# Kernel tuning notes

Measured on AMD Instinct MI355X. Metric: run time of the kernel, lower is better.

Reference implementation:

```python
import jax, jax.numpy as jnp
import numpy as np

B, T, D, H = 8, 1024, 512, 8
CH = D // H          # chunk_size = d_model // num_heads
PAD = 0              # pad_token_id
MAX_TRANS = 1024     # translen cap from source
NINF = float('-inf')


def setup_inputs() -> dict:
    key = jax.random.key(0)
    ks = jax.random.split(key, 8)
    features = jax.random.normal(ks[0], (B, T, D), jnp.float32)
    pos_embed = jax.random.normal(ks[1], (B, T, D), jnp.float32)
    tokens = jax.random.randint(ks[2], (B, T), 0, 32000, dtype=jnp.int32)
    Wq = jax.random.normal(ks[3], (D, 2 * D), jnp.float32) * 0.02
    bq = jnp.zeros((D,), jnp.float32)
    Wk = jax.random.normal(ks[4], (D, 2 * D), jnp.float32) * 0.02
    bk = jnp.zeros((D,), jnp.float32)
    Wg = jax.random.normal(ks[5], (H, 2 * D), jnp.float32) * 0.02
    bg = jnp.zeros((H,), jnp.float32)
    return dict(features=features, pos_embed=pos_embed, tokens=tokens,
                Wq=Wq, bq=bq, Wk=Wk, bk=bk, Wg=Wg, bg=bg)


def _safe_log_softmax(x, axis):
    # matches torch F.log_softmax followed by re-masking: rows that are all -inf stay -inf
    m = jnp.max(x, axis=axis, keepdims=True)
    allinf = jnp.isneginf(m)
    m_safe = jnp.where(allinf, 0.0, m)
    lse = m_safe + jnp.log(jnp.sum(jnp.exp(x - m_safe), axis=axis, keepdims=True))
    lse = jnp.where(allinf, 0.0, lse)
    return x - lse


def _safe_logsumexp(x, axis):
    # matches the custom logsumexp helper in the source (all -inf -> -inf, no nan)
    m = jnp.max(x, axis=axis)
    mask = jnp.isneginf(m)
    m_safe = jnp.where(mask, 0.0, m)
    s = jnp.sum(jnp.exp(x - jnp.expand_dims(m_safe, axis)), axis=axis)
    return jnp.log(jnp.where(mask, 1.0, s)) + jnp.where(mask, NINF, m_safe)


def reference(features, pos_embed, tokens, Wq, bq, Wk, bk, Wg, bg):
    # features_withpos = cat(decoder_out, link positional embedding)  -> [B, T, 2D]
    f = jnp.concatenate([features, pos_embed], axis=-1)
    q = (f @ Wq.T + bq).reshape(B, T, H, CH)
    k = (f @ Wk.T + bk).reshape(B, T, H, CH)
    log_gates = jax.nn.log_softmax(f @ Wg.T + bg, axis=-1)  # [B, T, H]
    # einsum 'bicf,bjcf->bijc' with c = head chunk
    scores = jnp.einsum('bihc,bjhc->bijh', q, k) / np.float32(np.sqrt(CH))  # [B,T,T,H]

    translen = min(MAX_TRANS, T - 1)
    n_valid = jnp.sum(tokens != PAD, axis=-1)  # [B]
    # banded indices: position i links to positions i+1 .. i+translen
    band_idx = jnp.arange(T)[:, None] + jnp.arange(translen)[None, :] + 1  # [T, translen]
    invalid = band_idx[None, :, :] >= n_valid[:, None, None]               # [B, T, translen]
    idx_c = jnp.where(invalid, 0, band_idx[None, :, :])
    idx_full = jnp.broadcast_to(idx_c[..., None], (B, T, translen, H))
    extract = jnp.take_along_axis(scores, idx_full, axis=2)                # [B,T,translen,H]
    extract = jnp.where(invalid[..., None], NINF, extract)
    # normalize over transition axis, then mask fully-invalid rows back to -inf
    extract = _safe_log_softmax(extract, axis=2)
    nouse = jnp.all(invalid, axis=-1)                                      # [B, T]
    extract = jnp.where(nouse[:, :, None, None], NINF, extract)
    # head-gated logsumexp over heads -> banded links [B, T, translen]
    links_band = _safe_logsumexp(extract + log_gates[:, :, None, :], axis=-1)
    # restore_valid_links: scatter band back to full [B, T, T] (-inf elsewhere)
    rel = jnp.arange(T)[None, :] - jnp.arange(T)[:, None] - 1              # [T, T]
    valid = (rel >= 0) & (rel < translen)
    rel_c = jnp.clip(rel, 0, translen - 1)
    rel_full = jnp.broadcast_to(rel_c[None, :, :], (B, T, T))
    out = jnp.take_along_axis(links_band, rel_full, axis=2)
    return jnp.where(valid[None, :, :], out, NINF)
```

## Files before the change

### kernel.cpp

```cpp
#include <hip/hip_runtime.h>
#include <math.h>

#define BATCH 8
#define T 1024
#define NH 8
#define NROW 8192
#define NEG_INF (-INFINITY)
#define SENT (-1.0e30f)
#define SC 0.180336880f
#define LOG2E 1.442695041f

typedef __attribute__((ext_vector_type(8))) short short8;
typedef __attribute__((ext_vector_type(4))) float f32x4;

__device__ __forceinline__ ushort f2bf(float x) {
  uint u = __float_as_uint(x);
  return (ushort)((u + 0x7FFFu + ((u >> 16) & 1u)) >> 16);
}
__device__ __forceinline__ uint pack2(float a, float b) {
  return (uint)f2bf(a) | ((uint)f2bf(b) << 16);
}
__device__ __forceinline__ void gl_lds16(const ushort* g, ushort* l) {
  __builtin_amdgcn_global_load_lds(
      (const __attribute__((address_space(1))) unsigned int*)g,
      (__attribute__((address_space(3))) unsigned int*)l, 16, 0, 0);
}

__global__ __launch_bounds__(256) void k_prep(
    const float* __restrict__ feat, const float* __restrict__ pos,
    const int* __restrict__ tokens,
    const float* __restrict__ Wq, const float* __restrict__ Wk,
    const float* __restrict__ Wg, const float* __restrict__ bg,
    ushort* __restrict__ fbf, ushort* __restrict__ Wbf,
    float* __restrict__ gout, int* __restrict__ nvout) {
  const int bid = blockIdx.x;
  const int tid = threadIdx.x;

  if (bid < 1024) {
    __shared__ __align__(16) float Ws[8192];
#pragma unroll
    for (int u = 0; u < 8; ++u)
      ((float4*)Ws)[u * 256 + tid] = ((const float4*)Wg)[u * 256 + tid];
    __syncthreads();

    const int w = tid >> 6, l = tid & 63;
    const int c0 = l * 16;
    const int row0 = bid * 8 + w * 2;

    float4 f[2][4];
#pragma unroll
    for (int r = 0; r < 2; ++r) {
      const int row = row0 + r;
      const float* src = (c0 < 512) ? (feat + (size_t)row * 512 + c0)
                                    : (pos + (size_t)row * 512 + (c0 - 512));
#pragma unroll
      for (int q4 = 0; q4 < 4; ++q4) f[r][q4] = *(const float4*)(src + q4 * 4);
      uint4 o0, o1;
      o0.x = pack2(f[r][0].x, f[r][0].y); o0.y = pack2(f[r][0].z, f[r][0].w);
      o0.z = pack2(f[r][1].x, f[r][1].y); o0.w = pack2(f[r][1].z, f[r][1].w);
      o1.x = pack2(f[r][2].x, f[r][2].y); o1.y = pack2(f[r][2].z, f[r][2].w);
      o1.z = pack2(f[r][3].x, f[r][3].y); o1.w = pack2(f[r][3].z, f[r][3].w);
      *(uint4*)(fbf + (size_t)row * 1024 + c0) = o0;
      *(uint4*)(fbf + (size_t)row * 1024 + c0 + 8) = o1;
    }

    float s[2][8];
#pragma unroll
    for (int h = 0; h < 8; ++h) {
      const float* wg = Ws + h * 1024 + c0;
      float4 w0 = *(const float4*)(wg + 0);
      float4 w1 = *(const float4*)(wg + 4);
      float4 w2 = *(const float4*)(wg + 8);
      float4 w3 = *(const float4*)(wg + 12);
#pragma unroll
      for (int r = 0; r < 2; ++r)
        s[r][h] = f[r][0].x * w0.x + f[r][0].y * w0.y + f[r][0].z * w0.z + f[r][0].w * w0.w
                + f[r][1].x * w1.x + f[r][1].y * w1.y + f[r][1].z * w1.z + f[r][1].w * w1.w
                + f[r][2].x * w2.x + f[r][2].y * w2.y + f[r][2].z * w2.z + f[r][2].w * w2.w
                + f[r][3].x * w3.x + f[r][3].y * w3.y + f[r][3].z * w3.z + f[r][3].w * w3.w;
    }
#pragma unroll
    for (int m = 1; m < 64; m <<= 1)
#pragma unroll
      for (int r = 0; r < 2; ++r)
#pragma unroll
        for (int h = 0; h < 8; ++h) s[r][h] += __shfl_xor(s[r][h], m, 64);
    if (l == 0) {
#pragma unroll
      for (int r = 0; r < 2; ++r) {
        float lg[8], mx = -1e30f;
#pragma unroll
        for (int h = 0; h < 8; ++h) { lg[h] = s[r][h] + bg[h]; mx = fmaxf(mx, lg[h]); }
        float sum = 0.f;
#pragma unroll
        for (int h = 0; h < 8; ++h) sum += __expf(lg[h] - mx);
        const float lse = mx + __logf(sum);
#pragma unroll
        for (int h = 0; h < 8; ++h) gout[(size_t)(row0 + r) * 8 + h] = lg[h] - lse;
      }
    }
  } else if (bid < 1536) {
    const int gid = (bid - 1024) * 256 + tid;
    const int e0 = gid * 8;
    const int n = e0 >> 10, k = e0 & 1023;
    const float* src = (n < 512) ? (Wq + (size_t)n * 1024 + k)
                                 : (Wk + (size_t)(n - 512) * 1024 + k);
    float4 a = *(const float4*)src;
    float4 b = *(const float4*)(src + 4);
    uint4 o;
    o.x = pack2(a.x, a.y); o.y = pack2(a.z, a.w);
    o.z = pack2(b.x, b.y); o.w = pack2(b.z, b.w);
    *(uint4*)(Wbf + (size_t)n * 1024 + k) = o;
  } else {
    const int b = bid - 1536;
    int cnt = 0;
    for (int i = tid; i < T; i += 256) cnt += (tokens[b * T + i] != 0) ? 1 : 0;
    __shared__ int s[256];
    s[tid] = cnt;
    __syncthreads();
    for (int st = 128; st > 0; st >>= 1) {
      if (tid < st) s[tid] += s[tid + st];
      __syncthreads();
    }
    if (tid == 0) nvout[b] = s[0];
  }
}

__global__ __launch_bounds__(256) void k_gemm(
    const ushort* __restrict__ fbf, const ushort* __restrict__ Wbf,
    const float* __restrict__ bq, const float* __restrict__ bk,
    ushort* __restrict__ qbuf, ushort* __restrict__ kbuf) {
  const int g = blockIdx.x + 8 * blockIdx.y;
  const int wid = (g & 7) * 64 + (g >> 3);
  const int n0 = (wid & 7) * 128;
  const int m0 = (wid >> 3) * 128;
  const int tid = threadIdx.x;
  const int w = tid >> 6, l = tid & 63;
  const int lo = l & 15, quad = l >> 4;
  const int wm0 = (w >> 1) * 64, wn0 = (w & 1) * 64;

  __shared__ ushort As[2][128 * 64];
  __shared__ ushort Bs[2][128 * 64];

  f32x4 acc[4][4];
#pragma unroll
  for (int i = 0; i < 4; ++i)
#pragma unroll
    for (int j = 0; j < 4; ++j) acc[i][j] = (f32x4){0.f, 0.f, 0.f, 0.f};

  const int c8 = (tid & 7) * 8;
  const int r0 = tid >> 3;

  auto stage = [&](int buf, int k0) {
#pragma unroll
    for (int u = 0; u < 4; ++u) {
      gl_lds16(fbf + (size_t)(m0 + u * 32 + r0) * 1024 + k0 + c8,
               As[buf] + (size_t)w * 512 + u * 2048);
      gl_lds16(Wbf + (size_t)(n0 + u * 32 + r0) * 1024 + k0 + c8,
               Bs[buf] + (size_t)w * 512 + u * 2048);
    }
  };

  stage(0, 0);
  int cur = 0;
  for (int k0 = 0; k0 < 1024; k0 += 64) {
    __syncthreads();
    if (k0 + 64 < 1024) stage(cur ^ 1, k0 + 64);
    const ushort* pA = As[cur];
    const ushort* pB = Bs[cur];
#pragma unroll
    for (int kk = 0; kk < 2; ++kk) {
      short8 af[4], bfr[4];
#pragma unroll
      for (int mi = 0; mi < 4; ++mi)
        af[mi] = *(const short8*)(pA + (size_t)(wm0 + mi * 16 + lo) * 64 + kk * 32 + quad * 8);
#pragma unroll
      for (int ni = 0; ni < 4; ++ni)
        bfr[ni] = *(const short8*)(pB + (size_t)(wn0 + ni * 16 + lo) * 64 + kk * 32 + quad * 8);
#pragma unroll
      for (int mi = 0; mi < 4; ++mi)
#pragma unroll
        for (int ni = 0; ni < 4; ++ni)
          acc[mi][ni] = __builtin_amdgcn_mfma_f32_16x16x32_bf16(bfr[ni], af[mi], acc[mi][ni], 0, 0, 0);
    }
    cur ^= 1;
  }

  float4 bias4[4];
#pragma unroll
  for (int ni = 0; ni < 4; ++ni) {
    const int gn = n0 + wn0 + ni * 16 + quad * 4;
    bias4[ni] = *(const float4*)((gn < 512) ? (bq + gn) : (bk + gn - 512));
  }
#pragma unroll
  for (int mi = 0; mi < 4; ++mi) {
    const int m = m0 + wm0 + mi * 16 + lo;
#pragma unroll
    for (int ni = 0; ni < 4; ++ni) {
      const int gn = n0 + wn0 + ni * 16 + quad * 4;
      ushort* dst = (gn < 512) ? (qbuf + (size_t)m * 512 + gn)
                               : (kbuf + (size_t)m * 512 + gn - 512);
      ushort4 o;
      o.x = f2bf(acc[mi][ni][0] + bias4[ni].x);
      o.y = f2bf(acc[mi][ni][1] + bias4[ni].y);
      o.z = f2bf(acc[mi][ni][2] + bias4[ni].z);
      o.w = f2bf(acc[mi][ni][3] + bias4[ni].w);
      *(ushort4*)dst = o;
    }
  }
}

__global__ __launch_bounds__(256) void k_pass1(
    const ushort* __restrict__ q, const ushort* __restrict__ kv,
    const float* __restrict__ g, const int* __restrict__ nvp,
    float* __restrict__ Wt) {
  const int it = blockIdx.x, h = blockIdx.y, b = blockIdx.z;
  const int nv = nvp[b];
  const int i0 = it * 64;
  const int tid = threadIdx.x;
  const int w = tid >> 6, l = tid & 63;
  const int lo = l & 15, quad = l >> 4;

  __shared__ ushort Ks[2][64 * 64];

  const int i = i0 + w * 16 + lo;
  const ushort* qp = q + (size_t)(b * T + i) * 512 + h * 64 + quad * 8;
  const short8 a0 = *(const short8*)qp;
  const short8 a1 = *(const short8*)(qp + 32);

  float lsum = 0.f;
  const int ntile = ((nv + 63) >> 6) - it;

  if (ntile > 0) {
    auto stage = [&](int buf, int jt) {
#pragma unroll
      for (int u = 0; u < 2; ++u) {
        const int s = u * 256 + tid;
        const int row = s >> 3, c = s & 7;
        gl_lds16(kv + (size_t)(b * T + jt * 64 + row) * 512 + h * 64 + ((c ^ (row & 7)) * 8),
                 Ks[buf] + (size_t)(u * 256 + w * 64) * 8);
      }
    };
    stage(0, it);
    __syncthreads();
    for (int s = 0; s < ntile; ++s) {
      if (s + 1 < ntile) stage((s + 1) & 1, it + s + 1);
      const ushort* kbase = Ks[s & 1];
      const int j0 = (it + s) * 64;
      const bool diag = (s == 0);
      const bool masked = diag | (j0 + 64 > nv);
#pragma unroll
      for (int ni = 0; ni < 4; ++ni) {
        if (diag && ni < w) continue;
        const int rw = ni * 16 + lo;
        const short8 b0 = *(const short8*)(kbase + (size_t)rw * 64 + ((quad ^ (rw & 7)) * 8));
        const short8 b1 = *(const short8*)(kbase + (size_t)rw * 64 + (((4 + quad) ^ (rw & 7)) * 8));
        f32x4 acc = (f32x4){0.f, 0.f, 0.f, 0.f};
        acc = __builtin_amdgcn_mfma_f32_16x16x32_bf16(b0, a0, acc, 0, 0, 0);
        acc = __builtin_amdgcn_mfma_f32_16x16x32_bf16(b1, a1, acc, 0, 0, 0);
        if (!masked) {
#pragma unroll
          for (int r = 0; r < 4; ++r) lsum += __builtin_amdgcn_exp2f(acc[r] * SC);
        } else {
          const int jb = j0 + ni * 16 + quad * 4;
#pragma unroll
          for (int r = 0; r < 4; ++r) {
            const int j = jb + r;
            if (j > i && j < nv) lsum += __builtin_amdgcn_exp2f(acc[r] * SC);
          }
        }
      }
      __syncthreads();
    }
  }

  lsum += __shfl_xor(lsum, 16, 64);
  lsum += __shfl_xor(lsum, 32, 64);
  if (quad == 0) {
    const size_t row = (size_t)(b * T) + i;
    Wt[(size_t)h * NROW + row] =
        (lsum > 0.f) ? (g[row * 8 + h] - __logf(lsum)) : NEG_INF;
  }
}

__global__ __launch_bounds__(256) void k_pass2(
    const ushort* __restrict__ q, const ushort* __restrict__ kv,
    const float* __restrict__ Wt, const int* __restrict__ nvp,
    float* __restrict__ out) {
  const int jt = blockIdx.x, it = blockIdx.y, b = blockIdx.z;
  const int nv = nvp[b];
  const int i0 = it * 64, j0 = jt * 64;
  const int tid = threadIdx.x;

  if (jt < it || j0 >= nv) {
    const int r0 = tid >> 4, c0 = (tid & 15) * 4;
    float4 v; v.x = v.y = v.z = v.w = SENT;
#pragma unroll
    for (int u = 0; u < 4; ++u)
      *(float4*)(out + ((size_t)(b * T + i0 + r0 + u * 16)) * T + j0 + c0) = v;
    return;
  }

  const int w = tid >> 6, l = tid & 63;
  const int lo = l & 15, quad = l >> 4;
  const int i = i0 + w * 16 + lo;

  __shared__ ushort Ks[2][64 * 64];

  auto stage = [&](int buf, int h) {
#pragma unroll
    for (int u = 0; u < 2; ++u) {
      const int s = u * 256 + tid;
      const int row = s >> 3, c = s & 7;
      gl_lds16(kv + (size_t)(b * T + j0 + row) * 512 + h * 64 + ((c ^ (row & 7)) * 8),
               Ks[buf] + (size_t)(u * 256 + w * 64) * 8);
    }
  };

  stage(0, 0);

  const ushort* qb = q + (size_t)(b * T + i) * 512 + quad * 8;
  short8 qa0[8], qa1[8];
  float wl[8];
#pragma unroll
  for (int h = 0; h < 8; ++h) {
    qa0[h] = *(const short8*)(qb + h * 64);
    qa1[h] = *(const short8*)(qb + h * 64 + 32);
    wl[h] = Wt[(size_t)h * NROW + b * T + i] * LOG2E;
  }

  float se[4][4];
#pragma unroll
  for (int a = 0; a < 4; ++a)
#pragma unroll
    for (int c = 0; c < 4; ++c) se[a][c] = 0.f;

  __syncthreads();

#pragma unroll
  for (int h = 0; h < 8; ++h) {
    if (h < 7) stage((h + 1) & 1, h + 1);
    const ushort* kbase = Ks[h & 1];
#pragma unroll
    for (int ni = 0; ni < 4; ++ni) {
      const int rw = ni * 16 + lo;
      const short8 b0 = *(const short8*)(kbase + (size_t)rw * 64 + ((quad ^ (rw & 7)) * 8));
      const short8 b1 = *(const short8*)(kbase + (size_t)rw * 64 + (((4 + quad) ^ (rw & 7)) * 8));
      f32x4 acc = (f32x4){0.f, 0.f, 0.f, 0.f};
      acc = __builtin_amdgcn_mfma_f32_16x16x32_bf16(b0, qa0[h], acc, 0, 0, 0);
      acc = __builtin_amdgcn_mfma_f32_16x16x32_bf16(b1, qa1[h], acc, 0, 0, 0);
#pragma unroll
      for (int r = 0; r < 4; ++r)
        se[ni][r] += __builtin_amdgcn_exp2f(acc[r] * SC + wl[h]);
    }
    if (h < 7) __syncthreads();
  }

  const size_t orow = ((size_t)(b * T + i)) * T;
#pragma unroll
  for (int ni = 0; ni < 4; ++ni) {
    const int jb = j0 + ni * 16 + quad * 4;
    float4 v;
    v.x = (jb + 0 > i && jb + 0 < nv) ? fmaxf(__logf(se[ni][0]), SENT) : SENT;
    v.y = (jb + 1 > i && jb + 1 < nv) ? fmaxf(__logf(se[ni][1]), SENT) : SENT;
    v.z = (jb + 2 > i && jb + 2 < nv) ? fmaxf(__logf(se[ni][2]), SENT) : SENT;
    v.w = (jb + 3 > i && jb + 3 < nv) ? fmaxf(__logf(se[ni][3]), SENT) : SENT;
    *(float4*)(out + orow + jb) = v;
  }
}

extern "C" void kernel_launch(void* const* d_in, const int* in_sizes, int n_in,
                              void* d_out, int out_size, void* d_ws, size_t ws_size,
                              hipStream_t stream) {
  (void)in_sizes; (void)n_in; (void)out_size; (void)ws_size;
  const float* feat = (const float*)d_in[0];
  const float* pos  = (const float*)d_in[1];
  const int* tokens = (const int*)d_in[2];
  const float* Wq = (const float*)d_in[3];
  const float* bq = (const float*)d_in[4];
  const float* Wk = (const float*)d_in[5];
  const float* bk = (const float*)d_in[6];
  const float* Wg = (const float*)d_in[7];
  const float* bg = (const float*)d_in[8];
  float* out = (float*)d_out;

  ushort* qbuf = (ushort*)d_ws;
  ushort* kbuf = qbuf + (size_t)NROW * 512;
  ushort* Wbf  = kbuf + (size_t)NROW * 512;
  float*  gbuf = (float*)(Wbf + (size_t)1024 * 1024);
  float*  Wt   = gbuf + (size_t)NROW * NH;
  int*    nv   = (int*)(Wt + (size_t)NH * NROW);

  ushort* fbf = (ushort*)d_out;

  k_prep<<<dim3(1544), dim3(256), 0, stream>>>(feat, pos, tokens, Wq, Wk, Wg, bg,
                                               fbf, Wbf, gbuf, nv);
  k_gemm<<<dim3(8, 64), dim3(256), 0, stream>>>(fbf, Wbf, bq, bk, qbuf, kbuf);
  k_pass1<<<dim3(16, NH, BATCH), dim3(256), 0, stream>>>(qbuf, kbuf, gbuf, nv, Wt);
  k_pass2<<<dim3(16, 16, BATCH), dim3(256), 0, stream>>>(qbuf, kbuf, Wt, nv, out);
}
```

Baseline: 182.5 us.

## Retile GEMM to 512 threads with swizzled LDS, widen pass2 tiles, reorder grids

The GEMM moves to 512 threads with 8 waves, each computing a 64x32 sub-tile, and adds an XOR swizzle on the LDS layout to avoid bank conflicts on fragment reads. Pass2 doubles the j-tile to 128 columns so each staged K tile and Q load serve more MFMAs. Q fragments are now loaded per head instead of being held for all eight heads, and an unmasked fast path handles the epilogue. Both attention grids put batch on the fastest-varying block index, which changes scheduling and load balance across the causal/valid region. The risks are more register pressure from se[8][4], coarser skipping of masked tiles, and more redundant work on diagonal tiles.

```diff
diff --git a/kernel.cpp b/kernel.cpp
--- a/kernel.cpp
+++ b/kernel.cpp
@@ -126,7 +126,7 @@
   }
 }
 
-__global__ __launch_bounds__(256) void k_gemm(
+__global__ __launch_bounds__(512, 4) void k_gemm(
     const ushort* __restrict__ fbf, const ushort* __restrict__ Wbf,
     const float* __restrict__ bq, const float* __restrict__ bk,
     ushort* __restrict__ qbuf, ushort* __restrict__ kbuf) {
@@ -137,27 +137,28 @@
   const int tid = threadIdx.x;
   const int w = tid >> 6, l = tid & 63;
   const int lo = l & 15, quad = l >> 4;
-  const int wm0 = (w >> 1) * 64, wn0 = (w & 1) * 64;
+  const int wm0 = (w >> 2) * 64;
+  const int wn0 = (w & 3) * 32;
 
   __shared__ ushort As[2][128 * 64];
   __shared__ ushort Bs[2][128 * 64];
 
-  f32x4 acc[4][4];
+  f32x4 acc[4][2];
 #pragma unroll
   for (int i = 0; i < 4; ++i)
 #pragma unroll
-    for (int j = 0; j < 4; ++j) acc[i][j] = (f32x4){0.f, 0.f, 0.f, 0.f};
-
-  const int c8 = (tid & 7) * 8;
+    for (int j = 0; j < 2; ++j) acc[i][j] = (f32x4){0.f, 0.f, 0.f, 0.f};
+
+  const int csw = ((tid & 7) ^ ((tid >> 3) & 7)) * 8;
   const int r0 = tid >> 3;
 
   auto stage = [&](int buf, int k0) {
 #pragma unroll
-    for (int u = 0; u < 4; ++u) {
-      gl_lds16(fbf + (size_t)(m0 + u * 32 + r0) * 1024 + k0 + c8,
-               As[buf] + (size_t)w * 512 + u * 2048);
-      gl_lds16(Wbf + (size_t)(n0 + u * 32 + r0) * 1024 + k0 + c8,
-               Bs[buf] + (size_t)w * 512 + u * 2048);
+    for (int u = 0; u < 2; ++u) {
+      gl_lds16(fbf + (size_t)(m0 + u * 64 + r0) * 1024 + k0 + csw,
+               As[buf] + (size_t)(u * 512 + w * 64) * 8);
+      gl_lds16(Wbf + (size_t)(n0 + u * 64 + r0) * 1024 + k0 + csw,
+               Bs[buf] + (size_t)(u * 512 + w * 64) * 8);
     }
   };
 
@@ -170,25 +171,26 @@
     const ushort* pB = Bs[cur];
 #pragma unroll
     for (int kk = 0; kk < 2; ++kk) {
-      short8 af[4], bfr[4];
+      const int swz = ((kk * 4 + quad) ^ (lo & 7)) * 8;
+      short8 af[4], bfr[2];
 #pragma unroll
       for (int mi = 0; mi < 4; ++mi)
-        af[mi] = *(const short8*)(pA + (size_t)(wm0 + mi * 16 + lo) * 64 + kk * 32 + quad * 8);
-#pragma unroll
-      for (int ni = 0; ni < 4; ++ni)
-        bfr[ni] = *(const short8*)(pB + (size_t)(wn0 + ni * 16 + lo) * 64 + kk * 32 + quad * 8);
+        af[mi] = *(const short8*)(pA + (size_t)(wm0 + mi * 16 + lo) * 64 + swz);
+#pragma unroll
+      for (int ni = 0; ni < 2; ++ni)
+        bfr[ni] = *(const short8*)(pB + (size_t)(wn0 + ni * 16 + lo) * 64 + swz);
 #pragma unroll
       for (int mi = 0; mi < 4; ++mi)
 #pragma unroll
-        for (int ni = 0; ni < 4; ++ni)
+        for (int ni = 0; ni < 2; ++ni)
           acc[mi][ni] = __builtin_amdgcn_mfma_f32_16x16x32_bf16(bfr[ni], af[mi], acc[mi][ni], 0, 0, 0);
     }
     cur ^= 1;
   }
 
-  float4 bias4[4];
-#pragma unroll
-  for (int ni = 0; ni < 4; ++ni) {
+  float4 bias4[2];
+#pragma unroll
+  for (int ni = 0; ni < 2; ++ni) {
     const int gn = n0 + wn0 + ni * 16 + quad * 4;
     bias4[ni] = *(const float4*)((gn < 512) ? (bq + gn) : (bk + gn - 512));
   }
@@ -196,7 +198,7 @@
   for (int mi = 0; mi < 4; ++mi) {
     const int m = m0 + wm0 + mi * 16 + lo;
 #pragma unroll
-    for (int ni = 0; ni < 4; ++ni) {
+    for (int ni = 0; ni < 2; ++ni) {
       const int gn = n0 + wn0 + ni * 16 + quad * 4;
       ushort* dst = (gn < 512) ? (qbuf + (size_t)m * 512 + gn)
                                : (kbuf + (size_t)m * 512 + gn - 512);
@@ -214,7 +216,7 @@
     const ushort* __restrict__ q, const ushort* __restrict__ kv,
     const float* __restrict__ g, const int* __restrict__ nvp,
     float* __restrict__ Wt) {
-  const int it = blockIdx.x, h = blockIdx.y, b = blockIdx.z;
+  const int b = blockIdx.x, h = blockIdx.y, it = blockIdx.z;
   const int nv = nvp[b];
   const int i0 = it * 64;
   const int tid = threadIdx.x;
@@ -287,53 +289,49 @@
     const ushort* __restrict__ q, const ushort* __restrict__ kv,
     const float* __restrict__ Wt, const int* __restrict__ nvp,
     float* __restrict__ out) {
-  const int jt = blockIdx.x, it = blockIdx.y, b = blockIdx.z;
+  const int b = blockIdx.x, jt = blockIdx.y, it = blockIdx.z;
   const int nv = nvp[b];
-  const int i0 = it * 64, j0 = jt * 64;
+  const int i0 = it * 64, j0 = jt * 128;
   const int tid = threadIdx.x;
 
-  if (jt < it || j0 >= nv) {
-    const int r0 = tid >> 4, c0 = (tid & 15) * 4;
+  if (j0 + 127 <= i0 || j0 >= nv) {
+    const int r0 = tid >> 5, c0 = (tid & 31) * 4;
     float4 v; v.x = v.y = v.z = v.w = SENT;
 #pragma unroll
-    for (int u = 0; u < 4; ++u)
-      *(float4*)(out + ((size_t)(b * T + i0 + r0 + u * 16)) * T + j0 + c0) = v;
+    for (int u = 0; u < 8; ++u)
+      *(float4*)(out + ((size_t)(b * T + i0 + r0 + u * 8)) * T + j0 + c0) = v;
     return;
   }
 
-  const int w = tid >> 6, l = tid & 63;
+  const int wv = tid >> 6, l = tid & 63;
   const int lo = l & 15, quad = l >> 4;
-  const int i = i0 + w * 16 + lo;
-
-  __shared__ ushort Ks[2][64 * 64];
+  const int i = i0 + wv * 16 + lo;
+
+  __shared__ ushort Ks[2][128 * 64];
 
   auto stage = [&](int buf, int h) {
 #pragma unroll
-    for (int u = 0; u < 2; ++u) {
+    for (int u = 0; u < 4; ++u) {
       const int s = u * 256 + tid;
       const int row = s >> 3, c = s & 7;
       gl_lds16(kv + (size_t)(b * T + j0 + row) * 512 + h * 64 + ((c ^ (row & 7)) * 8),
-               Ks[buf] + (size_t)(u * 256 + w * 64) * 8);
+               Ks[buf] + (size_t)(u * 256 + wv * 64) * 8);
     }
   };
 
   stage(0, 0);
 
   const ushort* qb = q + (size_t)(b * T + i) * 512 + quad * 8;
-  short8 qa0[8], qa1[8];
   float wl[8];
 #pragma unroll
-  for (int h = 0; h < 8; ++h) {
-    qa0[h] = *(const short8*)(qb + h * 64);
-    qa1[h] = *(const short8*)(qb + h * 64 + 32);
+  for (int h = 0; h < 8; ++h)
     wl[h] = Wt[(size_t)h * NROW + b * T + i] * LOG2E;
-  }
-
-  float se[4][4];
-#pragma unroll
-  for (int a = 0; a < 4; ++a)
-#pragma unroll
-    for (int c = 0; c < 4; ++c) se[a][c] = 0.f;
+
+  float se[8][4];
+#pragma unroll
+  for (int a = 0; a < 8; ++a)
+#pragma unroll
+    for (int r = 0; r < 4; ++r) se[a][r] = 0.f;
 
   __syncthreads();
 
@@ -341,14 +339,16 @@
   for (int h = 0; h < 8; ++h) {
     if (h < 7) stage((h + 1) & 1, h + 1);
     const ushort* kbase = Ks[h & 1];
-#pragma unroll
-    for (int ni = 0; ni < 4; ++ni) {
+    const short8 a0 = *(const short8*)(qb + h * 64);
+    const short8 a1 = *(const short8*)(qb + h * 64 + 32);
+#pragma unroll
+    for (int ni = 0; ni < 8; ++ni) {
       const int rw = ni * 16 + lo;
       const short8 b0 = *(const short8*)(kbase + (size_t)rw * 64 + ((quad ^ (rw & 7)) * 8));
       const short8 b1 = *(const short8*)(kbase + (size_t)rw * 64 + (((4 + quad) ^ (rw & 7)) * 8));
       f32x4 acc = (f32x4){0.f, 0.f, 0.f, 0.f};
-      acc = __builtin_amdgcn_mfma_f32_16x16x32_bf16(b0, qa0[h], acc, 0, 0, 0);
-      acc = __builtin_amdgcn_mfma_f32_16x16x32_bf16(b1, qa1[h], acc, 0, 0, 0);
+      acc = __builtin_amdgcn_mfma_f32_16x16x32_bf16(b0, a0, acc, 0, 0, 0);
+      acc = __builtin_amdgcn_mfma_f32_16x16x32_bf16(b1, a1, acc, 0, 0, 0);
 #pragma unroll
       for (int r = 0; r < 4; ++r)
         se[ni][r] += __builtin_amdgcn_exp2f(acc[r] * SC + wl[h]);
@@ -357,15 +357,29 @@
   }
 
   const size_t orow = ((size_t)(b * T + i)) * T;
-#pragma unroll
-  for (int ni = 0; ni < 4; ++ni) {
-    const int jb = j0 + ni * 16 + quad * 4;
-    float4 v;
-    v.x = (jb + 0 > i && jb + 0 < nv) ? fmaxf(__logf(se[ni][0]), SENT) : SENT;
-    v.y = (jb + 1 > i && jb + 1 < nv) ? fmaxf(__logf(se[ni][1]), SENT) : SENT;
-    v.z = (jb + 2 > i && jb + 2 < nv) ? fmaxf(__logf(se[ni][2]), SENT) : SENT;
-    v.w = (jb + 3 > i && jb + 3 < nv) ? fmaxf(__logf(se[ni][3]), SENT) : SENT;
-    *(float4*)(out + orow + jb) = v;
+  const bool maskfree = (j0 >= i0 + 64) && (j0 + 128 <= nv);
+  if (maskfree) {
+#pragma unroll
+    for (int ni = 0; ni < 8; ++ni) {
+      const int jb = j0 + ni * 16 + quad * 4;
+      float4 v;
+      v.x = fmaxf(__logf(se[ni][0]), SENT);
+      v.y = fmaxf(__logf(se[ni][1]), SENT);
+      v.z = fmaxf(__logf(se[ni][2]), SENT);
+      v.w = fmaxf(__logf(se[ni][3]), SENT);
+      *(float4*)(out + orow + jb) = v;
+    }
+  } else {
+#pragma unroll
+    for (int ni = 0; ni < 8; ++ni) {
+      const int jb = j0 + ni * 16 + quad * 4;
+      float4 v;
+      v.x = (jb + 0 > i && jb + 0 < nv) ? fmaxf(__logf(se[ni][0]), SENT) : SENT;
+      v.y = (jb + 1 > i && jb + 1 < nv) ? fmaxf(__logf(se[ni][1]), SENT) : SENT;
+      v.z = (jb + 2 > i && jb + 2 < nv) ? fmaxf(__logf(se[ni][2]), SENT) : SENT;
+      v.w = (jb + 3 > i && jb + 3 < nv) ? fmaxf(__logf(se[ni][3]), SENT) : SENT;
+      *(float4*)(out + orow + jb) = v;
+    }
   }
 }
 
@@ -395,7 +409,7 @@
 
   k_prep<<<dim3(1544), dim3(256), 0, stream>>>(feat, pos, tokens, Wq, Wk, Wg, bg,
                                                fbf, Wbf, gbuf, nv);
-  k_gemm<<<dim3(8, 64), dim3(256), 0, stream>>>(fbf, Wbf, bq, bk, qbuf, kbuf);
-  k_pass1<<<dim3(16, NH, BATCH), dim3(256), 0, stream>>>(qbuf, kbuf, gbuf, nv, Wt);
-  k_pass2<<<dim3(16, 16, BATCH), dim3(256), 0, stream>>>(qbuf, kbuf, Wt, nv, out);
-}
+  k_gemm<<<dim3(8, 64), dim3(512), 0, stream>>>(fbf, Wbf, bq, bk, qbuf, kbuf);
+  k_pass1<<<dim3(BATCH, NH, 16), dim3(256), 0, stream>>>(qbuf, kbuf, gbuf, nv, Wt);
+  k_pass2<<<dim3(BATCH, 8, 16), dim3(256), 0, stream>>>(qbuf, kbuf, Wt, nv, out);
+}
```

Measured after the change: 157.7 us. 1.16x faster.
